# Performance work log

Measured on AMD Instinct MI355X. Metric: run time of the kernel, lower is better.

The kernel has to match this reference:

```python
import jax, jax.numpy as jnp
import numpy as np

WS = 8
NH = 6

def setup_inputs() -> dict:
    key = jax.random.key(0)
    ks = jax.random.split(key, 6)
    B, H, W, C = 4, 256, 256, 192
    return {
        "x": jax.random.normal(ks[0], (B, H * W, C), dtype=jnp.float32),
        "qkv_w": jax.random.normal(ks[1], (3 * C, C), dtype=jnp.float32) * 0.02,
        "qkv_b": jax.random.normal(ks[2], (3 * C,), dtype=jnp.float32) * 0.02,
        "proj_w": jax.random.normal(ks[3], (C, C), dtype=jnp.float32) * 0.02,
        "proj_b": jax.random.normal(ks[4], (C,), dtype=jnp.float32) * 0.02,
        "bias": jax.random.normal(ks[5], (NH, WS * WS, WS * WS), dtype=jnp.float32) * 0.02,
        "H": H,
        "W": W,
    }

def reference(x, qkv_w, qkv_b, proj_w, proj_b, bias, H, W):
    B, L, C = x.shape
    ws, nh = WS, NH
    hd = C // nh
    scale = hd ** -0.5
    H_pad = (H + ws - 1) // ws * ws
    W_pad = (W + ws - 1) // ws * ws
    pad_b, pad_r = H_pad - H, W_pad - W
    xv = x.reshape(B, H, W, C)
    if pad_b > 0 or pad_r > 0:
        xv = jnp.pad(xv, ((0, 0), (0, pad_b), (0, pad_r), (0, 0)))
    nHw, nWw = H_pad // ws, W_pad // ws
    # window partition: [B*nH*nW, ws*ws, C]
    xw = xv.reshape(B, nHw, ws, nWw, ws, C).transpose(0, 1, 3, 2, 4, 5)
    xw = xw.reshape(B * nHw * nWw, ws * ws, C)
    qkv = xw @ qkv_w.T + qkv_b  # [Bw, ws*ws, 3C]
    qkv = qkv.reshape(-1, ws * ws, 3, nh, hd).transpose(2, 0, 3, 1, 4)
    q, k, v = qkv[0], qkv[1], qkv[2]  # each [Bw, nh, ws*ws, hd]
    attn = jnp.einsum('bhqd,bhkd->bhqk', q * scale, k) + bias
    attn = jax.nn.softmax(attn, axis=-1)
    out = jnp.einsum('bhqk,bhkd->bhqd', attn, v)
    out = out.transpose(0, 2, 1, 3).reshape(-1, ws * ws, C)
    out = out @ proj_w.T + proj_b
    # window reverse: [B, H_pad, W_pad, C]
    out = out.reshape(B, nHw, nWw, ws, ws, C).transpose(0, 1, 3, 2, 4, 5)
    out = out.reshape(B, H_pad, W_pad, C)
    if pad_b > 0 or pad_r > 0:
        out = out[:, :H, :W, :]
    return out.reshape(B, H * W, C)
```

## Files before the change

### kernel.cpp

```cpp
#include <hip/hip_runtime.h>

typedef short bf16x8 __attribute__((ext_vector_type(8)));
typedef float f32x4 __attribute__((ext_vector_type(4)));

#define QKV_FRAG_SH 110592
#define PROJ_FRAG_SH 36864
#define EBIAS_OFF_B 294912
#define SCALE 0.17677669529663689f
#define SMEM_BYTES 158720

__device__ __forceinline__ short f2bf(float f) {
  unsigned x = __float_as_uint(f);
  x = (x + 0x7FFFu + ((x >> 16) & 1u)) >> 16;
  return (short)x;
}

__global__ void cvt_w(const float* __restrict__ qkv_w,
                      const float* __restrict__ proj_w,
                      const float* __restrict__ bias,
                      short* __restrict__ wfrag,
                      float* __restrict__ ebias) {
  int idx = blockIdx.x * 256 + threadIdx.x;
  if (idx < QKV_FRAG_SH) {
    int j = idx & 7, lane = (idx >> 3) & 63, t = idx >> 9;
    int nt = t / 6, ks = t - nt * 6;
    int n0 = nt * 16 + (lane & 15);
    float v = qkv_w[n0 * 192 + ks * 32 + (lane >> 4) * 8 + j];
    if (n0 < 192) v *= SCALE;
    wfrag[idx] = f2bf(v);
  } else if (idx < QKV_FRAG_SH + PROJ_FRAG_SH) {
    int i2 = idx - QKV_FRAG_SH;
    int j = i2 & 7, lane = (i2 >> 3) & 63, t = i2 >> 9;
    int nt = t / 6, ks = t - nt * 6;
    wfrag[idx] = f2bf(proj_w[(nt * 16 + (lane & 15)) * 192 + ks * 32 + (lane >> 4) * 8 + j]);
  } else {
    int i3 = idx - (QKV_FRAG_SH + PROJ_FRAG_SH);
    ebias[i3] = __expf(bias[i3]);
  }
}

__global__ __launch_bounds__(512, 2) void swin_fused(
    const float* __restrict__ x,
    const float* __restrict__ qkv_b,
    const float* __restrict__ proj_b,
    const short* __restrict__ wfrag,
    const float* __restrict__ ebias,
    float* __restrict__ out) {
  extern __shared__ short smem[];
  short* buf = smem;
  short* q_l = smem + 25600;
  short* k_l = smem + 40960;
  short* v_l = smem + 56320;
  short* p_s = smem + 70144;

  const short* wq = wfrag;
  const short* wp = wfrag + QKV_FRAG_SH;

  const int tid = threadIdx.x;
  const int w = tid >> 6, lane = tid & 63, quad = lane >> 4, lm = lane & 15;
  const int m = w & 3;

  int goff[6], loff[6];
  #pragma unroll
  for (int i = 0; i < 6; ++i) {
    int idx4 = tid + i * 512;
    int chunk = idx4 / 384;
    int off = idx4 - chunk * 384;
    goff[i] = chunk * 49152 + off * 4;
    loff[i] = (chunk * 8 + off / 48) * 200 + (off % 48) * 4;
  }

  size_t base;
  {
    int wid = blockIdx.x;
    int b = wid >> 10, rem = wid & 1023, wh = rem >> 5, ww = rem & 31;
    base = ((size_t)b * 65536 + (size_t)(wh * 8) * 256 + (size_t)(ww * 8)) * 192;
    const float* xp = x + base;
    #pragma unroll
    for (int i = 0; i < 6; ++i) {
      float4 f = *(const float4*)(xp + goff[i]);
      short4 s = { f2bf(f.x), f2bf(f.y), f2bf(f.z), f2bf(f.w) };
      *(short4*)&buf[loff[i]] = s;
    }
  }
  __syncthreads();

  float4 pf[6];
  size_t nbase = 0;
  #pragma unroll 1
  for (int it = 0; it < 16; ++it) {
    const int cur = (it & 1) * 12800;
    const int nxt = 12800 - cur;

    if (it < 15) {
      int wid = (it + 1) * 256 + blockIdx.x;
      int b = wid >> 10, rem = wid & 1023, wh = rem >> 5, ww = rem & 31;
      nbase = ((size_t)b * 65536 + (size_t)(wh * 8) * 256 + (size_t)(ww * 8)) * 192;
      const float* xp = x + nbase;
      #pragma unroll
      for (int i = 0; i < 6; ++i) pf[i] = *(const float4*)(xp + goff[i]);
    }

    {
      bf16x8 af[6];
      #pragma unroll
      for (int ks = 0; ks < 6; ++ks)
        af[ks] = *(const bf16x8*)&buf[cur + (m * 16 + lm) * 200 + ks * 32 + quad * 8];
      const int nt0 = (w >> 2) * 18;
      for (int ntl = 0; ntl < 18; ++ntl) {
        int nt = nt0 + ntl;
        f32x4 acc = {0.f, 0.f, 0.f, 0.f};
        #pragma unroll
        for (int ks = 0; ks < 6; ++ks) {
          bf16x8 bw = *(const bf16x8*)&wq[((nt * 6 + ks) * 64 + lane) * 8];
          acc = __builtin_amdgcn_mfma_f32_16x16x32_bf16(af[ks], bw, acc, 0, 0, 0);
        }
        float bn = qkv_b[nt * 16 + lm];
        if (nt < 12) {
          bn *= SCALE;
          int h = nt >> 1, dh = nt & 1;
          int rb = h * 64 + m * 16 + quad * 4;
          #pragma unroll
          for (int r = 0; r < 4; ++r)
            q_l[(rb + r) * 40 + dh * 16 + lm] = f2bf(acc[r] + bn);
        } else if (nt < 24) {
          int h = (nt - 12) >> 1, dh = nt & 1;
          int rb = h * 64 + m * 16 + quad * 4;
          #pragma unroll
          for (int r = 0; r < 4; ++r)
            k_l[(rb + r) * 40 + dh * 16 + lm] = f2bf(acc[r] + bn);
        } else {
          int h = (nt - 24) >> 1, dh = nt & 1;
          short4 s4 = { f2bf(acc[0] + bn), f2bf(acc[1] + bn),
                        f2bf(acc[2] + bn), f2bf(acc[3] + bn) };
          *(short4*)&v_l[(h * 32 + dh * 16 + lm) * 72 + m * 16 + quad * 4] = s4;
        }
      }
    }
    __syncthreads();

    if (it < 15) {
      #pragma unroll
      for (int i = 0; i < 6; ++i) {
        short4 s = { f2bf(pf[i].x), f2bf(pf[i].y), f2bf(pf[i].z), f2bf(pf[i].w) };
        *(short4*)&buf[nxt + loff[i]] = s;
      }
    }

    {
      const int pb = w * 1152;
      #pragma unroll 1
      for (int i = 0; i < 3; ++i) {
        int tk = w + i * 8;
        int h = tk >> 2, mt = tk & 3;
        float eb[4][4];
        const float* ebp = ebias + h * 4096 + (mt * 16 + quad * 4) * 64 + lm;
        #pragma unroll
        for (int nt = 0; nt < 4; ++nt)
          #pragma unroll
          for (int r = 0; r < 4; ++r)
            eb[nt][r] = ebp[r * 64 + nt * 16];
        bf16x8 aq = *(const bf16x8*)&q_l[(h * 64 + mt * 16 + lm) * 40 + quad * 8];
        f32x4 lg[4];
        #pragma unroll
        for (int nt = 0; nt < 4; ++nt) {
          bf16x8 bk = *(const bf16x8*)&k_l[(h * 64 + nt * 16 + lm) * 40 + quad * 8];
          f32x4 z = {0.f, 0.f, 0.f, 0.f};
          lg[nt] = __builtin_amdgcn_mfma_f32_16x16x32_bf16(aq, bk, z, 0, 0, 0);
        }
        float s[4] = {0.f, 0.f, 0.f, 0.f};
        #pragma unroll
        for (int r = 0; r < 4; ++r) {
          #pragma unroll
          for (int nt = 0; nt < 4; ++nt) {
            float e = __expf(lg[nt][r]) * eb[nt][r];
            s[r] += e;
            p_s[pb + (quad * 4 + r) * 72 + nt * 16 + lm] = f2bf(e);
          }
        }
        #pragma unroll
        for (int r = 0; r < 4; ++r) {
          s[r] += __shfl_xor(s[r], 1);
          s[r] += __shfl_xor(s[r], 2);
          s[r] += __shfl_xor(s[r], 4);
          s[r] += __shfl_xor(s[r], 8);
        }
        asm volatile("s_waitcnt lgkmcnt(0)" ::: "memory");
        f32x4 o0 = {0.f,0.f,0.f,0.f}, o1 = {0.f,0.f,0.f,0.f};
        #pragma unroll
        for (int ks = 0; ks < 2; ++ks) {
          bf16x8 ap  = *(const bf16x8*)&p_s[pb + lm * 72 + ks * 32 + quad * 8];
          bf16x8 bv0 = *(const bf16x8*)&v_l[(h * 32 + lm) * 72 + ks * 32 + quad * 8];
          bf16x8 bv1 = *(const bf16x8*)&v_l[(h * 32 + 16 + lm) * 72 + ks * 32 + quad * 8];
          o0 = __builtin_amdgcn_mfma_f32_16x16x32_bf16(ap, bv0, o0, 0, 0, 0);
          o1 = __builtin_amdgcn_mfma_f32_16x16x32_bf16(ap, bv1, o1, 0, 0, 0);
        }
        #pragma unroll
        for (int r = 0; r < 4; ++r) {
          float ir = 1.0f / s[r];
          int rowo = cur + (mt * 16 + quad * 4 + r) * 200 + h * 32;
          buf[rowo + lm]      = f2bf(o0[r] * ir);
          buf[rowo + 16 + lm] = f2bf(o1[r] * ir);
        }
      }
    }
    __syncthreads();

    {
      bf16x8 af2[6];
      #pragma unroll
      for (int ks = 0; ks < 6; ++ks)
        af2[ks] = *(const bf16x8*)&buf[cur + (m * 16 + lm) * 200 + ks * 32 + quad * 8];
      const int nt0 = (w >> 2) * 6;
      #pragma unroll 1
      for (int ntl = 0; ntl < 6; ++ntl) {
        int nt = nt0 + ntl;
        f32x4 acc = {0.f, 0.f, 0.f, 0.f};
        #pragma unroll
        for (int ks = 0; ks < 6; ++ks) {
          bf16x8 bw = *(const bf16x8*)&wp[((nt * 6 + ks) * 64 + lane) * 8];
          acc = __builtin_amdgcn_mfma_f32_16x16x32_bf16(af2[ks], bw, acc, 0, 0, 0);
        }
        float pbv = proj_b[nt * 16 + lm];
        #pragma unroll
        for (int r = 0; r < 4; ++r) {
          int t = m * 16 + quad * 4 + r;
          out[base + (size_t)((t >> 3) * 256 + (t & 7)) * 192 + nt * 16 + lm] = acc[r] + pbv;
        }
      }
    }
    base = nbase;
  }
}

extern "C" void kernel_launch(void* const* d_in, const int* in_sizes, int n_in,
                              void* d_out, int out_size, void* d_ws, size_t ws_size,
                              hipStream_t stream) {
  const float* x      = (const float*)d_in[0];
  const float* qkv_w  = (const float*)d_in[1];
  const float* qkv_b  = (const float*)d_in[2];
  const float* proj_w = (const float*)d_in[3];
  const float* proj_b = (const float*)d_in[4];
  const float* bias   = (const float*)d_in[5];
  short* wfrag = (short*)d_ws;
  float* ebias = (float*)((char*)d_ws + EBIAS_OFF_B);

  hipFuncSetAttribute((const void*)swin_fused,
                      hipFuncAttributeMaxDynamicSharedMemorySize, SMEM_BYTES);

  hipLaunchKernelGGL(cvt_w, dim3(672), dim3(256), 0, stream,
                     qkv_w, proj_w, bias, wfrag, ebias);
  hipLaunchKernelGGL(swin_fused, dim3(256), dim3(512), SMEM_BYTES, stream,
                     x, qkv_b, proj_b, wfrag, ebias, (float*)d_out);
}
```

Measured before the change: 603.4 us.

## Use 12 waves per block and fold bias into MFMA accumulator with exp2

Raises the block size from 512 to 768 threads (12 waves), splitting the QKV, attention and projection work over three wave groups instead of two, with matching load partitioning. The relative-position bias is pre-scaled by log2(e) and loaded as the initial MFMA accumulator, and the exponent becomes exp2f, which removes the separate multiply by exp(bias). Q/K row stride shrinks from 40 to 36 to fit the larger p_s scratch in shared memory. The 768-thread blocks with a 3-blocks-per-SM launch bound tighten the register budget per thread and can change LDS bank-conflict patterns.

Result: faster. 573.1 us (-5.0%).

```diff
diff --git a/kernel.cpp b/kernel.cpp
--- a/kernel.cpp
+++ b/kernel.cpp
@@ -5,9 +5,11 @@
 
 #define QKV_FRAG_SH 110592
 #define PROJ_FRAG_SH 36864
-#define EBIAS_OFF_B 294912
+#define BIAS2_OFF_B 294912
 #define SCALE 0.17677669529663689f
-#define SMEM_BYTES 158720
+#define LOG2E 1.44269504088896341f
+#define QSCALE (SCALE * LOG2E)
+#define SMEM_BYTES 161792
 
 __device__ __forceinline__ short f2bf(float f) {
   unsigned x = __float_as_uint(f);
@@ -19,14 +21,14 @@
                       const float* __restrict__ proj_w,
                       const float* __restrict__ bias,
                       short* __restrict__ wfrag,
-                      float* __restrict__ ebias) {
+                      float* __restrict__ bias2) {
   int idx = blockIdx.x * 256 + threadIdx.x;
   if (idx < QKV_FRAG_SH) {
     int j = idx & 7, lane = (idx >> 3) & 63, t = idx >> 9;
     int nt = t / 6, ks = t - nt * 6;
     int n0 = nt * 16 + (lane & 15);
     float v = qkv_w[n0 * 192 + ks * 32 + (lane >> 4) * 8 + j];
-    if (n0 < 192) v *= SCALE;
+    if (n0 < 192) v *= QSCALE;
     wfrag[idx] = f2bf(v);
   } else if (idx < QKV_FRAG_SH + PROJ_FRAG_SH) {
     int i2 = idx - QKV_FRAG_SH;
@@ -35,35 +37,35 @@
     wfrag[idx] = f2bf(proj_w[(nt * 16 + (lane & 15)) * 192 + ks * 32 + (lane >> 4) * 8 + j]);
   } else {
     int i3 = idx - (QKV_FRAG_SH + PROJ_FRAG_SH);
-    ebias[i3] = __expf(bias[i3]);
-  }
-}
-
-__global__ __launch_bounds__(512, 2) void swin_fused(
+    bias2[i3] = bias[i3] * LOG2E;
+  }
+}
+
+__global__ __launch_bounds__(768, 3) void swin_fused(
     const float* __restrict__ x,
     const float* __restrict__ qkv_b,
     const float* __restrict__ proj_b,
     const short* __restrict__ wfrag,
-    const float* __restrict__ ebias,
+    const float* __restrict__ bias2,
     float* __restrict__ out) {
   extern __shared__ short smem[];
   short* buf = smem;
   short* q_l = smem + 25600;
-  short* k_l = smem + 40960;
-  short* v_l = smem + 56320;
-  short* p_s = smem + 70144;
+  short* k_l = smem + 39424;
+  short* v_l = smem + 53248;
+  short* p_s = smem + 67072;
 
   const short* wq = wfrag;
   const short* wp = wfrag + QKV_FRAG_SH;
 
   const int tid = threadIdx.x;
   const int w = tid >> 6, lane = tid & 63, quad = lane >> 4, lm = lane & 15;
-  const int m = w & 3;
-
-  int goff[6], loff[6];
+  const int m = w & 3, g = w >> 2;
+
+  int goff[4], loff[4];
   #pragma unroll
-  for (int i = 0; i < 6; ++i) {
-    int idx4 = tid + i * 512;
+  for (int i = 0; i < 4; ++i) {
+    int idx4 = tid + i * 768;
     int chunk = idx4 / 384;
     int off = idx4 - chunk * 384;
     goff[i] = chunk * 49152 + off * 4;
@@ -77,7 +79,7 @@
     base = ((size_t)b * 65536 + (size_t)(wh * 8) * 256 + (size_t)(ww * 8)) * 192;
     const float* xp = x + base;
     #pragma unroll
-    for (int i = 0; i < 6; ++i) {
+    for (int i = 0; i < 4; ++i) {
       float4 f = *(const float4*)(xp + goff[i]);
       short4 s = { f2bf(f.x), f2bf(f.y), f2bf(f.z), f2bf(f.w) };
       *(short4*)&buf[loff[i]] = s;
@@ -85,7 +87,7 @@
   }
   __syncthreads();
 
-  float4 pf[6];
+  float4 pf[4];
   size_t nbase = 0;
   #pragma unroll 1
   for (int it = 0; it < 16; ++it) {
@@ -98,7 +100,7 @@
       nbase = ((size_t)b * 65536 + (size_t)(wh * 8) * 256 + (size_t)(ww * 8)) * 192;
       const float* xp = x + nbase;
       #pragma unroll
-      for (int i = 0; i < 6; ++i) pf[i] = *(const float4*)(xp + goff[i]);
+      for (int i = 0; i < 4; ++i) pf[i] = *(const float4*)(xp + goff[i]);
     }
 
     {
@@ -106,8 +108,8 @@
       #pragma unroll
       for (int ks = 0; ks < 6; ++ks)
         af[ks] = *(const bf16x8*)&buf[cur + (m * 16 + lm) * 200 + ks * 32 + quad * 8];
-      const int nt0 = (w >> 2) * 18;
-      for (int ntl = 0; ntl < 18; ++ntl) {
+      const int nt0 = g * 12;
+      for (int ntl = 0; ntl < 12; ++ntl) {
         int nt = nt0 + ntl;
         f32x4 acc = {0.f, 0.f, 0.f, 0.f};
         #pragma unroll
@@ -117,18 +119,18 @@
         }
         float bn = qkv_b[nt * 16 + lm];
         if (nt < 12) {
-          bn *= SCALE;
+          bn *= QSCALE;
           int h = nt >> 1, dh = nt & 1;
           int rb = h * 64 + m * 16 + quad * 4;
           #pragma unroll
           for (int r = 0; r < 4; ++r)
-            q_l[(rb + r) * 40 + dh * 16 + lm] = f2bf(acc[r] + bn);
+            q_l[(rb + r) * 36 + dh * 16 + lm] = f2bf(acc[r] + bn);
         } else if (nt < 24) {
           int h = (nt - 12) >> 1, dh = nt & 1;
           int rb = h * 64 + m * 16 + quad * 4;
           #pragma unroll
           for (int r = 0; r < 4; ++r)
-            k_l[(rb + r) * 40 + dh * 16 + lm] = f2bf(acc[r] + bn);
+            k_l[(rb + r) * 36 + dh * 16 + lm] = f2bf(acc[r] + bn);
         } else {
           int h = (nt - 24) >> 1, dh = nt & 1;
           short4 s4 = { f2bf(acc[0] + bn), f2bf(acc[1] + bn),
@@ -141,7 +143,7 @@
 
     if (it < 15) {
       #pragma unroll
-      for (int i = 0; i < 6; ++i) {
+      for (int i = 0; i < 4; ++i) {
         short4 s = { f2bf(pf[i].x), f2bf(pf[i].y), f2bf(pf[i].z), f2bf(pf[i].w) };
         *(short4*)&buf[nxt + loff[i]] = s;
       }
@@ -150,30 +152,30 @@
     {
       const int pb = w * 1152;
       #pragma unroll 1
-      for (int i = 0; i < 3; ++i) {
-        int tk = w + i * 8;
+      for (int i = 0; i < 2; ++i) {
+        int tk = w + i * 12;
         int h = tk >> 2, mt = tk & 3;
-        float eb[4][4];
-        const float* ebp = ebias + h * 4096 + (mt * 16 + quad * 4) * 64 + lm;
-        #pragma unroll
-        for (int nt = 0; nt < 4; ++nt)
-          #pragma unroll
-          for (int r = 0; r < 4; ++r)
-            eb[nt][r] = ebp[r * 64 + nt * 16];
-        bf16x8 aq = *(const bf16x8*)&q_l[(h * 64 + mt * 16 + lm) * 40 + quad * 8];
+        const float* bp = bias2 + h * 4096 + (mt * 16 + quad * 4) * 64 + lm;
         f32x4 lg[4];
         #pragma unroll
         for (int nt = 0; nt < 4; ++nt) {
-          bf16x8 bk = *(const bf16x8*)&k_l[(h * 64 + nt * 16 + lm) * 40 + quad * 8];
-          f32x4 z = {0.f, 0.f, 0.f, 0.f};
-          lg[nt] = __builtin_amdgcn_mfma_f32_16x16x32_bf16(aq, bk, z, 0, 0, 0);
+          lg[nt][0] = bp[nt * 16];
+          lg[nt][1] = bp[nt * 16 + 64];
+          lg[nt][2] = bp[nt * 16 + 128];
+          lg[nt][3] = bp[nt * 16 + 192];
+        }
+        bf16x8 aq = *(const bf16x8*)&q_l[(h * 64 + mt * 16 + lm) * 36 + quad * 8];
+        #pragma unroll
+        for (int nt = 0; nt < 4; ++nt) {
+          bf16x8 bk = *(const bf16x8*)&k_l[(h * 64 + nt * 16 + lm) * 36 + quad * 8];
+          lg[nt] = __builtin_amdgcn_mfma_f32_16x16x32_bf16(aq, bk, lg[nt], 0, 0, 0);
         }
         float s[4] = {0.f, 0.f, 0.f, 0.f};
         #pragma unroll
         for (int r = 0; r < 4; ++r) {
           #pragma unroll
           for (int nt = 0; nt < 4; ++nt) {
-            float e = __expf(lg[nt][r]) * eb[nt][r];
+            float e = exp2f(lg[nt][r]);
             s[r] += e;
             p_s[pb + (quad * 4 + r) * 72 + nt * 16 + lm] = f2bf(e);
           }
@@ -211,9 +213,9 @@
       #pragma unroll
       for (int ks = 0; ks < 6; ++ks)
         af2[ks] = *(const bf16x8*)&buf[cur + (m * 16 + lm) * 200 + ks * 32 + quad * 8];
-      const int nt0 = (w >> 2) * 6;
+      const int nt0 = g * 4;
       #pragma unroll 1
-      for (int ntl = 0; ntl < 6; ++ntl) {
+      for (int ntl = 0; ntl < 4; ++ntl) {
         int nt = nt0 + ntl;
         f32x4 acc = {0.f, 0.f, 0.f, 0.f};
         #pragma unroll
@@ -243,13 +245,13 @@
   const float* proj_b = (const float*)d_in[4];
   const float* bias   = (const float*)d_in[5];
   short* wfrag = (short*)d_ws;
-  float* ebias = (float*)((char*)d_ws + EBIAS_OFF_B);
+  float* bias2 = (float*)((char*)d_ws + BIAS2_OFF_B);
 
   hipFuncSetAttribute((const void*)swin_fused,
                       hipFuncAttributeMaxDynamicSharedMemorySize, SMEM_BYTES);
 
   hipLaunchKernelGGL(cvt_w, dim3(672), dim3(256), 0, stream,
-                     qkv_w, proj_w, bias, wfrag, ebias);
-  hipLaunchKernelGGL(swin_fused, dim3(256), dim3(512), SMEM_BYTES, stream,
-                     x, qkv_b, proj_b, wfrag, ebias, (float*)d_out);
-}
+                     qkv_w, proj_w, bias, wfrag, bias2);
+  hipLaunchKernelGGL(swin_fused, dim3(256), dim3(768), SMEM_BYTES, stream,
+                     x, qkv_b, proj_b, wfrag, bias2, (float*)d_out);
+}
```
